# Kernel tuning notes

Hardware: AMD Instinct MI355X
Metric: run time of the kernel (lower is better)

Reference implementation:

```python
import jax, jax.numpy as jnp
import numpy as np

N_CLAUSES = 200000
N_FEATURES = 64
HIDDEN = 128
N_STEPS = 512


def setup_inputs() -> dict:
    key = jax.random.key(0)
    ks = jax.random.split(key, 8)
    features = jax.random.normal(ks[0], (N_CLAUSES, N_FEATURES), jnp.float32)
    W1 = jax.random.normal(ks[1], (N_FEATURES, HIDDEN), jnp.float32) / np.sqrt(N_FEATURES)
    b1 = jnp.zeros((HIDDEN,), jnp.float32)
    W2 = jax.random.normal(ks[2], (HIDDEN, HIDDEN), jnp.float32) / np.sqrt(HIDDEN)
    b2 = jnp.zeros((HIDDEN,), jnp.float32)
    key_w = jax.random.normal(ks[3], (HIDDEN,), jnp.float32) / np.sqrt(HIDDEN)
    # sel_mask[s, n] = clause n is in the passive set at SEL step s
    sel_mask = jax.random.bernoulli(ks[4], 0.5, (N_STEPS, N_CLAUSES))
    # proof_mask[n] = clause n participates in the final proof (sparse)
    proof_mask = jax.random.bernoulli(ks[5], 0.02, (N_CLAUSES,))
    # guarantee passive & proof nonempty at every step (torch code divides by its size)
    proof_mask = proof_mask.at[0].set(True)
    sel_mask = sel_mask.at[:, 0].set(True)
    return {
        "features": features, "W1": W1, "b1": b1, "W2": W2, "b2": b2,
        "key_w": key_w, "sel_mask": sel_mask, "proof_mask": proof_mask,
    }


def reference(features, W1, b1, W2, b2, key_w, sel_mask, proof_mask):
    # clause_embedder: 2-layer MLP; clause_key: dot with key vector -> one logit per clause
    h = jax.nn.relu(features @ W1 + b1)          # [N, H]
    emb = h @ W2 + b2                            # [N, H]
    logits = emb @ key_w                         # [N]

    neg = jnp.finfo(logits.dtype).min
    masked = jnp.where(sel_mask, logits[None, :], neg)   # [S, N]
    lse = jax.nn.logsumexp(masked, axis=1)                # [S] log-softmax denominator over passive set

    tgt = sel_mask & proof_mask[None, :]                  # [S, N] passive & proof
    cnt = tgt.sum(axis=1).astype(logits.dtype)            # [S] (>=1 by construction)
    # soft-target CE: -sum_j t_j * log_softmax(logits)_j, t uniform over tgt
    num = jnp.where(tgt, logits[None, :], 0.0).sum(axis=1) / cnt
    loss = (lse - num).mean()                             # mean over SEL steps
    return loss
```

## Files before the change

kernel.cpp:

```cpp
#include <hip/hip_runtime.h>
#include <hip/hip_bf16.h>

#define DEV __device__ __forceinline__

constexpr int NC = 200000;
constexpr int NF = 64;
constexpr int NH = 128;
constexpr int NS = 512;

constexpr int OF_CFG   = 0;
constexpr int OF_W1    = 16;
constexpr int OF_B1    = OF_W1 + NF * NH;
constexpr int OF_W2K   = OF_B1 + NH;
constexpr int OF_B2K   = OF_W2K + NH;
constexpr int OF_MAX   = OF_B2K + 1;
constexpr int OF_ACCE  = OF_MAX + 1;
constexpr int OF_ACCP  = OF_ACCE + NS;
constexpr int OF_ACCC  = OF_ACCP + NS;
constexpr int OF_LOGIT = 16384;
constexpr int OF_E     = OF_LOGIT + NC;
constexpr int OF_PL    = OF_E + NC;
constexpr int OF_PC    = OF_PL + NC;

DEV float bf2f(unsigned short u) { return __uint_as_float(((unsigned)u) << 16); }

DEV float loadF(const void* p, int i, int fk) {
    return fk ? bf2f(((const unsigned short*)p)[i]) : ((const float*)p)[i];
}

DEV unsigned flipf(float x) {
    unsigned u = __float_as_uint(x);
    return (u & 0x80000000u) ? ~u : (u | 0x80000000u);
}
DEV float unflipf(unsigned u) {
    unsigned b = (u & 0x80000000u) ? (u ^ 0x80000000u) : ~u;
    return __uint_as_float(b);
}

DEV bool okhalf(unsigned h) { return h == 0u || h == 1u || h == 0x3F80u || h == 0x3C00u; }

__global__ void k_probe(const void* features, const void* W1, const void* b1,
                        const void* W2, const void* b2, const void* keyw,
                        const void* sel, float* ws) {
    __shared__ int s_tiny, s_w4, s_w2;
    __shared__ float kw[NH];
    __shared__ float pr[NH];
    int tx = threadIdx.x;
    if (tx == 0) { s_tiny = 0; s_w4 = 1; s_w2 = 1; }
    __syncthreads();
    {
        const unsigned short* u = (const unsigned short*)features;
        unsigned e = (u[tx] >> 7) & 0xFFu;
        if (e < 100u) atomicAdd(&s_tiny, 1);
        const unsigned* w = (const unsigned*)sel;
        unsigned v = w[tx];
        if (!(v == 0u || v == 1u || v == 0x3F800000u)) atomicAnd(&s_w4, 0);
        if (!(okhalf(v & 0xFFFFu) && okhalf(v >> 16))) atomicAnd(&s_w2, 0);
    }
    __syncthreads();
    int fk = (s_tiny >= 8) ? 0 : 1;
    int mw = s_w4 ? 4 : (s_w2 ? 2 : 1);
    if (tx == 0) { ((int*)ws)[0] = fk; ((int*)ws)[1] = mw; }
    if (tx < NH) kw[tx] = loadF(keyw, tx, fk);
    for (int i = tx; i < NF * NH; i += blockDim.x) {
        int f = i >> 7;
        int j = i & (NH - 1);
        int jc = j >> 2, c = j & 3;
        ws[OF_W1 + ((jc * NF + f) << 2) + c] = loadF(W1, i, fk);
    }
    if (tx < NH) ws[OF_B1 + tx] = loadF(b1, tx, fk);
    __syncthreads();
    if (tx < NH) {
        float s = 0.f;
        for (int k = 0; k < NH; k++) s += loadF(W2, tx * NH + k, fk) * kw[k];
        ws[OF_W2K + tx] = s;
        pr[tx] = loadF(b2, tx, fk) * kw[tx];
    }
    __syncthreads();
    if (tx == 0) {
        float s = 0.f;
        for (int k = 0; k < NH; k++) s += pr[k];
        ws[OF_B2K] = s;
        ((unsigned*)ws)[OF_MAX] = 0u;
    }
    for (int i = tx; i < 3 * NS; i += blockDim.x) ws[OF_ACCE + i] = 0.f;
}

__global__ __launch_bounds__(256) void k_logits(const void* features,
                                                const float* __restrict__ w1t,
                                                const float* __restrict__ bias1,
                                                const float* __restrict__ wk,
                                                const float* __restrict__ cfg,
                                                float* __restrict__ logits,
                                                unsigned* __restrict__ maxp) {
    __shared__ float sred[4];
    int tx = threadIdx.x;
    int fk = ((const int*)cfg)[0];
    float b2k = cfg[OF_B2K];
    int n = blockIdx.x * 256 + tx;
    float acc = -3.0e38f;
    if (n < NC) {
        float feat[NF];
        if (fk) {
            const uint4* fp = (const uint4*)((const unsigned short*)features + (size_t)n * NF);
            #pragma unroll
            for (int q = 0; q < 8; q++) {
                uint4 v = fp[q];
                unsigned vv[4] = {v.x, v.y, v.z, v.w};
                #pragma unroll
                for (int h = 0; h < 4; h++) {
                    feat[q * 8 + h * 2 + 0] = __uint_as_float(vv[h] << 16);
                    feat[q * 8 + h * 2 + 1] = __uint_as_float(vv[h] & 0xFFFF0000u);
                }
            }
        } else {
            const float4* fp = (const float4*)((const float*)features + (size_t)n * NF);
            #pragma unroll
            for (int q = 0; q < 16; q++) {
                float4 v = fp[q];
                feat[q * 4 + 0] = v.x; feat[q * 4 + 1] = v.y;
                feat[q * 4 + 2] = v.z; feat[q * 4 + 3] = v.w;
            }
        }
        acc = b2k;
        for (int jc = 0; jc < NH / 4; jc++) {
            const float4* wp = (const float4*)(w1t + (size_t)jc * (NF * 4));
            float4 b = *(const float4*)(bias1 + jc * 4);
            float d0 = b.x, d1 = b.y, d2 = b.z, d3 = b.w;
            #pragma unroll
            for (int f = 0; f < NF; f++) {
                float4 w = wp[f];
                d0 += feat[f] * w.x; d1 += feat[f] * w.y;
                d2 += feat[f] * w.z; d3 += feat[f] * w.w;
            }
            float4 k4 = *(const float4*)(wk + jc * 4);
            acc += fmaxf(d0, 0.f) * k4.x + fmaxf(d1, 0.f) * k4.y
                 + fmaxf(d2, 0.f) * k4.z + fmaxf(d3, 0.f) * k4.w;
        }
        logits[n] = acc;
    }
    float m = acc;
    #pragma unroll
    for (int k = 1; k < 64; k <<= 1) m = fmaxf(m, __shfl_xor(m, k, 64));
    if ((tx & 63) == 0) sred[tx >> 6] = m;
    __syncthreads();
    if (tx == 0) {
        m = fmaxf(fmaxf(sred[0], sred[1]), fmaxf(sred[2], sred[3]));
        atomicMax(maxp, flipf(m));
    }
}

__global__ void k_prep(const void* proof, float* ws) {
    int n = blockIdx.x * 256 + threadIdx.x;
    if (n >= NC) return;
    int mw = ((const int*)ws)[1];
    float M = unflipf(((const unsigned*)ws)[OF_MAX]);
    float l = ws[OF_LOGIT + n];
    ws[OF_E + n] = __expf(l - M);
    bool pf;
    if (mw == 1)      pf = ((const unsigned char*)proof)[n] != 0;
    else if (mw == 2) pf = ((const unsigned short*)proof)[n] != 0;
    else              pf = ((const unsigned*)proof)[n] != 0;
    ws[OF_PL + n] = pf ? l : 0.f;
    ws[OF_PC + n] = pf ? 1.f : 0.f;
}

constexpr int NT_N = 16;
constexpr int BL_N = 256 * NT_N;
constexpr int SG = 32;

template<int MW>
DEV void bloop(const void* sel, int s0, int baddr,
               const float (&e)[NT_N], const float (&pl)[NT_N], const float (&pc)[NT_N],
               float* ws) {
    for (int si = 0; si < SG; si++) {
        int s = s0 + si;
        size_t off = (size_t)s * NC + (size_t)baddr;
        float m[NT_N];
        if (MW == 1) {
            uint4 w = *(const uint4*)((const unsigned char*)sel + off);
            unsigned v[4] = {w.x, w.y, w.z, w.w};
            #pragma unroll
            for (int q = 0; q < 4; q++)
                #pragma unroll
                for (int b = 0; b < 4; b++)
                    m[q * 4 + b] = ((v[q] >> (8 * b)) & 0xFFu) ? 1.f : 0.f;
        } else if (MW == 2) {
            const uint4* p = (const uint4*)((const unsigned short*)sel + off);
            #pragma unroll
            for (int h = 0; h < 2; h++) {
                uint4 w = p[h];
                unsigned v[4] = {w.x, w.y, w.z, w.w};
                #pragma unroll
                for (int q = 0; q < 4; q++) {
                    m[h * 8 + q * 2 + 0] = (v[q] & 0xFFFFu) ? 1.f : 0.f;
                    m[h * 8 + q * 2 + 1] = (v[q] >> 16) ? 1.f : 0.f;
                }
            }
        } else {
            const uint4* p = (const uint4*)((const unsigned*)sel + off);
            #pragma unroll
            for (int q = 0; q < 4; q++) {
                uint4 w = p[q];
                m[q * 4 + 0] = w.x ? 1.f : 0.f; m[q * 4 + 1] = w.y ? 1.f : 0.f;
                m[q * 4 + 2] = w.z ? 1.f : 0.f; m[q * 4 + 3] = w.w ? 1.f : 0.f;
            }
        }
        float se = 0.f, sp = 0.f, sc = 0.f;
        #pragma unroll
        for (int i = 0; i < NT_N; i++) {
            se += m[i] * e[i]; sp += m[i] * pl[i]; sc += m[i] * pc[i];
        }
        #pragma unroll
        for (int k = 1; k < 64; k <<= 1) {
            se += __shfl_xor(se, k, 64);
            sp += __shfl_xor(sp, k, 64);
            sc += __shfl_xor(sc, k, 64);
        }
        if ((threadIdx.x & 63) == 0) {
            atomicAdd(&ws[OF_ACCE + s], se);
            atomicAdd(&ws[OF_ACCP + s], sp);
            atomicAdd(&ws[OF_ACCC + s], sc);
        }
    }
}

__global__ __launch_bounds__(256) void k_phaseB(const void* sel, float* ws) {
    int tx = threadIdx.x;
    int base = blockIdx.x * BL_N + tx * NT_N;
    int s0 = blockIdx.y * SG;
    bool active = base < NC;
    int baddr = active ? base : 0;
    float e[NT_N], pl[NT_N], pc[NT_N];
    #pragma unroll
    for (int q = 0; q < 4; q++) {
        float4 ve = active ? ((const float4*)&ws[OF_E + baddr])[q]  : make_float4(0, 0, 0, 0);
        float4 vp = active ? ((const float4*)&ws[OF_PL + baddr])[q] : make_float4(0, 0, 0, 0);
        float4 vc = active ? ((const float4*)&ws[OF_PC + baddr])[q] : make_float4(0, 0, 0, 0);
        e[q * 4 + 0] = ve.x; e[q * 4 + 1] = ve.y; e[q * 4 + 2] = ve.z; e[q * 4 + 3] = ve.w;
        pl[q * 4 + 0] = vp.x; pl[q * 4 + 1] = vp.y; pl[q * 4 + 2] = vp.z; pl[q * 4 + 3] = vp.w;
        pc[q * 4 + 0] = vc.x; pc[q * 4 + 1] = vc.y; pc[q * 4 + 2] = vc.z; pc[q * 4 + 3] = vc.w;
    }
    int mw = ((const int*)ws)[1];
    if (mw == 1)      bloop<1>(sel, s0, baddr, e, pl, pc, ws);
    else if (mw == 2) bloop<2>(sel, s0, baddr, e, pl, pc, ws);
    else              bloop<4>(sel, s0, baddr, e, pl, pc, ws);
}

__global__ void k_final(float* ws, void* out) {
    __shared__ float sred[256];
    int tx = threadIdx.x;
    float M = unflipf(((const unsigned*)ws)[OF_MAX]);
    float sum = 0.f;
    for (int s = tx; s < NS; s += 256) {
        float lse = M + logf(ws[OF_ACCE + s]);
        sum += lse - ws[OF_ACCP + s] / ws[OF_ACCC + s];
    }
    sred[tx] = sum;
    __syncthreads();
    for (int k = 128; k > 0; k >>= 1) {
        if (tx < k) sred[tx] += sred[tx + k];
        __syncthreads();
    }
    if (tx == 0) {
        float loss = sred[0] / (float)NS;
        int fk = ((const int*)ws)[0];
        if (fk) ((__hip_bfloat16*)out)[0] = __float2bfloat16(loss);
        else    ((float*)out)[0] = loss;
    }
}

extern "C" void kernel_launch(void* const* d_in, const int* in_sizes, int n_in,
                              void* d_out, int out_size, void* d_ws, size_t ws_size,
                              hipStream_t stream) {
    const void* features = d_in[0];
    const void* W1   = d_in[1];
    const void* b1   = d_in[2];
    const void* W2   = d_in[3];
    const void* b2   = d_in[4];
    const void* keyw = d_in[5];
    const void* sel  = d_in[6];
    const void* proof = d_in[7];
    float* ws = (float*)d_ws;

    k_probe<<<1, 256, 0, stream>>>(features, W1, b1, W2, b2, keyw, sel, ws);
    int nblk = (NC + 255) / 256;
    k_logits<<<nblk, 256, 0, stream>>>(features, ws + OF_W1, ws + OF_B1, ws + OF_W2K,
                                       ws, ws + OF_LOGIT, (unsigned*)ws + OF_MAX);
    k_prep<<<nblk, 256, 0, stream>>>(proof, ws);
    dim3 gB((NC + BL_N - 1) / BL_N, NS / SG);
    k_phaseB<<<gB, 256, 0, stream>>>(sel, ws);
    k_final<<<1, 256, 0, stream>>>(ws, d_out);
}
```

Measured before the change: 699.9 us.

## Use bf16 MFMA for logits MLP and fuse prep into phase-B kernel

When features arrive as bf16, the first layer now runs on MFMA 16x16x32 bf16 instructions using a pre-swizzled W1 layout prepared in the probe kernel. Bias, ReLU and the W2·key projection are applied in the epilogue. The separate prep kernel is removed, so exp(logit-M) and the proof-mask terms are computed inside the phase-B kernel and the intermediate arrays are no longer written and reread. SG doubles to 64 steps per block, which halves how often per-block setup runs at the cost of fewer blocks. The fp32 fallback path is kept but only 64 of 256 threads work, and its bounds handling for the last block looks fragile.

```diff
diff --git a/kernel.cpp b/kernel.cpp
--- a/kernel.cpp
+++ b/kernel.cpp
@@ -7,6 +7,9 @@
 constexpr int NF = 64;
 constexpr int NH = 128;
 constexpr int NS = 512;
+
+typedef __attribute__((ext_vector_type(8))) short short8;
+typedef __attribute__((ext_vector_type(4))) float f32x4;
 
 constexpr int OF_CFG   = 0;
 constexpr int OF_W1    = 16;
@@ -17,17 +20,13 @@
 constexpr int OF_ACCE  = OF_MAX + 1;
 constexpr int OF_ACCP  = OF_ACCE + NS;
 constexpr int OF_ACCC  = OF_ACCP + NS;
+constexpr int OF_EPT   = OF_ACCC + NS;
 constexpr int OF_LOGIT = 16384;
-constexpr int OF_E     = OF_LOGIT + NC;
-constexpr int OF_PL    = OF_E + NC;
-constexpr int OF_PC    = OF_PL + NC;
 
 DEV float bf2f(unsigned short u) { return __uint_as_float(((unsigned)u) << 16); }
-
 DEV float loadF(const void* p, int i, int fk) {
     return fk ? bf2f(((const unsigned short*)p)[i]) : ((const float*)p)[i];
 }
-
 DEV unsigned flipf(float x) {
     unsigned u = __float_as_uint(x);
     return (u & 0x80000000u) ? ~u : (u | 0x80000000u);
@@ -36,7 +35,6 @@
     unsigned b = (u & 0x80000000u) ? (u ^ 0x80000000u) : ~u;
     return __uint_as_float(b);
 }
-
 DEV bool okhalf(unsigned h) { return h == 0u || h == 1u || h == 0x3F80u || h == 0x3C00u; }
 
 __global__ void k_probe(const void* features, const void* W1, const void* b1,
@@ -44,7 +42,7 @@
                         const void* sel, float* ws) {
     __shared__ int s_tiny, s_w4, s_w2;
     __shared__ float kw[NH];
-    __shared__ float pr[NH];
+    __shared__ float part[256];
     int tx = threadIdx.x;
     if (tx == 0) { s_tiny = 0; s_w4 = 1; s_w2 = 1; }
     __syncthreads();
@@ -62,112 +60,141 @@
     int mw = s_w4 ? 4 : (s_w2 ? 2 : 1);
     if (tx == 0) { ((int*)ws)[0] = fk; ((int*)ws)[1] = mw; }
     if (tx < NH) kw[tx] = loadF(keyw, tx, fk);
-    for (int i = tx; i < NF * NH; i += blockDim.x) {
-        int f = i >> 7;
-        int j = i & (NH - 1);
-        int jc = j >> 2, c = j & 3;
-        ws[OF_W1 + ((jc * NF + f) << 2) + c] = loadF(W1, i, fk);
+    if (fk) {
+        const unsigned short* w1u = (const unsigned short*)W1;
+        unsigned short* dstp = (unsigned short*)(ws + OF_W1);
+        for (int i = tx; i < NF * NH; i += blockDim.x) {
+            int k = i >> 7, col = i & 127;
+            int t = col >> 4, c = col & 15;
+            int ks = k >> 5, kr = k & 31, q = kr >> 3, j = kr & 7;
+            dstp[(((t * 2 + ks) * 64) + q * 16 + c) * 8 + j] = w1u[i];
+        }
+    } else {
+        for (int i = tx; i < NF * NH; i += blockDim.x) {
+            int f = i >> 7, j = i & (NH - 1);
+            int jc = j >> 2, c = j & 3;
+            ws[OF_W1 + ((jc * NF + f) << 2) + c] = loadF(W1, i, fk);
+        }
     }
     if (tx < NH) ws[OF_B1 + tx] = loadF(b1, tx, fk);
     __syncthreads();
-    if (tx < NH) {
+    {
+        int row = tx >> 1, half = tx & 1;
         float s = 0.f;
-        for (int k = 0; k < NH; k++) s += loadF(W2, tx * NH + k, fk) * kw[k];
-        ws[OF_W2K + tx] = s;
-        pr[tx] = loadF(b2, tx, fk) * kw[tx];
-    }
+        for (int k = half * 64; k < half * 64 + 64; k++)
+            s += loadF(W2, row * NH + k, fk) * kw[k];
+        part[tx] = s;
+    }
+    __syncthreads();
+    if (tx < NH) ws[OF_W2K + tx] = part[2 * tx] + part[2 * tx + 1];
+    __syncthreads();
+    if (tx < NH) part[tx] = loadF(b2, tx, fk) * kw[tx];
     __syncthreads();
     if (tx == 0) {
         float s = 0.f;
-        for (int k = 0; k < NH; k++) s += pr[k];
+        for (int k = 0; k < NH; k++) s += part[k];
         ws[OF_B2K] = s;
         ((unsigned*)ws)[OF_MAX] = 0u;
     }
+    __syncthreads();
+    if (tx < 128) {
+        int c = tx >> 3, t = tx & 7;
+        ws[OF_EPT + 2 * tx + 0] = ws[OF_B1 + 16 * t + c];
+        ws[OF_EPT + 2 * tx + 1] = ws[OF_W2K + 16 * t + c];
+    }
     for (int i = tx; i < 3 * NS; i += blockDim.x) ws[OF_ACCE + i] = 0.f;
 }
 
 __global__ __launch_bounds__(256) void k_logits(const void* features,
-                                                const float* __restrict__ w1t,
-                                                const float* __restrict__ bias1,
-                                                const float* __restrict__ wk,
-                                                const float* __restrict__ cfg,
+                                                const float* __restrict__ wsro,
                                                 float* __restrict__ logits,
                                                 unsigned* __restrict__ maxp) {
-    __shared__ float sred[4];
     int tx = threadIdx.x;
-    int fk = ((const int*)cfg)[0];
-    float b2k = cfg[OF_B2K];
-    int n = blockIdx.x * 256 + tx;
-    float acc = -3.0e38f;
-    if (n < NC) {
-        float feat[NF];
-        if (fk) {
-            const uint4* fp = (const uint4*)((const unsigned short*)features + (size_t)n * NF);
-            #pragma unroll
-            for (int q = 0; q < 8; q++) {
-                uint4 v = fp[q];
-                unsigned vv[4] = {v.x, v.y, v.z, v.w};
+    int fk = ((const int*)wsro)[0];
+    float b2k = wsro[OF_B2K];
+    if (fk) {
+        int wv = tx >> 6, l = tx & 63;
+        int m = l & 15, q = l >> 4;
+        int n0 = blockIdx.x * 64 + wv * 16;
+        const unsigned short* fb = (const unsigned short*)features + (size_t)n0 * NF;
+        short8 a0 = *(const short8*)(fb + m * NF + q * 8);
+        short8 a1 = *(const short8*)(fb + m * NF + q * 8 + 32);
+        const short8* bf = (const short8*)(const void*)(wsro + OF_W1);
+        f32x4 acc[8];
+        #pragma unroll
+        for (int t = 0; t < 8; t++) {
+            f32x4 z = {0.f, 0.f, 0.f, 0.f};
+            short8 b0 = bf[(t * 2 + 0) * 64 + l];
+            short8 b1f = bf[(t * 2 + 1) * 64 + l];
+            z = __builtin_amdgcn_mfma_f32_16x16x32_bf16(a0, b0, z, 0, 0, 0);
+            z = __builtin_amdgcn_mfma_f32_16x16x32_bf16(a1, b1f, z, 0, 0, 0);
+            acc[t] = z;
+        }
+        const float2* ep = (const float2*)(const void*)(wsro + OF_EPT) + m * 8;
+        float p[4] = {0.f, 0.f, 0.f, 0.f};
+        #pragma unroll
+        for (int t = 0; t < 8; t++) {
+            float2 bw = ep[t];
+            #pragma unroll
+            for (int r = 0; r < 4; r++)
+                p[r] += fmaxf(acc[t][r] + bw.x, 0.f) * bw.y;
+        }
+        #pragma unroll
+        for (int k = 1; k < 16; k <<= 1)
+            #pragma unroll
+            for (int r = 0; r < 4; r++) p[r] += __shfl_xor(p[r], k, 64);
+        float mx = -3.0e38f;
+        if (m == 0) {
+            float4 o;
+            o.x = p[0] + b2k; o.y = p[1] + b2k; o.z = p[2] + b2k; o.w = p[3] + b2k;
+            *(float4*)(logits + n0 + q * 4) = o;
+            mx = fmaxf(fmaxf(o.x, o.y), fmaxf(o.z, o.w));
+        }
+        #pragma unroll
+        for (int k = 1; k < 64; k <<= 1) mx = fmaxf(mx, __shfl_xor(mx, k, 64));
+        if (l == 0) atomicMax(maxp, flipf(mx));
+    } else {
+        const float* w1t = wsro + OF_W1;
+        const float* bias1 = wsro + OF_B1;
+        const float* wk = wsro + OF_W2K;
+        float acc = -3.0e38f;
+        int n = blockIdx.x * 64 + tx;
+        if (tx < 64 && n < NC) {
+            float feat[NF];
+            const float4* fp = (const float4*)((const float*)features + (size_t)n * NF);
+            #pragma unroll
+            for (int qq = 0; qq < 16; qq++) {
+                float4 v = fp[qq];
+                feat[qq * 4 + 0] = v.x; feat[qq * 4 + 1] = v.y;
+                feat[qq * 4 + 2] = v.z; feat[qq * 4 + 3] = v.w;
+            }
+            acc = b2k;
+            for (int jc = 0; jc < NH / 4; jc++) {
+                const float4* wp = (const float4*)(w1t + (size_t)jc * (NF * 4));
+                float4 b = *(const float4*)(bias1 + jc * 4);
+                float d0 = b.x, d1 = b.y, d2 = b.z, d3 = b.w;
                 #pragma unroll
-                for (int h = 0; h < 4; h++) {
-                    feat[q * 8 + h * 2 + 0] = __uint_as_float(vv[h] << 16);
-                    feat[q * 8 + h * 2 + 1] = __uint_as_float(vv[h] & 0xFFFF0000u);
+                for (int f = 0; f < NF; f++) {
+                    float4 w = wp[f];
+                    d0 += feat[f] * w.x; d1 += feat[f] * w.y;
+                    d2 += feat[f] * w.z; d3 += feat[f] * w.w;
                 }
-            }
-        } else {
-            const float4* fp = (const float4*)((const float*)features + (size_t)n * NF);
-            #pragma unroll
-            for (int q = 0; q < 16; q++) {
-                float4 v = fp[q];
-                feat[q * 4 + 0] = v.x; feat[q * 4 + 1] = v.y;
-                feat[q * 4 + 2] = v.z; feat[q * 4 + 3] = v.w;
-            }
-        }
-        acc = b2k;
-        for (int jc = 0; jc < NH / 4; jc++) {
-            const float4* wp = (const float4*)(w1t + (size_t)jc * (NF * 4));
-            float4 b = *(const float4*)(bias1 + jc * 4);
-            float d0 = b.x, d1 = b.y, d2 = b.z, d3 = b.w;
-            #pragma unroll
-            for (int f = 0; f < NF; f++) {
-                float4 w = wp[f];
-                d0 += feat[f] * w.x; d1 += feat[f] * w.y;
-                d2 += feat[f] * w.z; d3 += feat[f] * w.w;
-            }
-            float4 k4 = *(const float4*)(wk + jc * 4);
-            acc += fmaxf(d0, 0.f) * k4.x + fmaxf(d1, 0.f) * k4.y
-                 + fmaxf(d2, 0.f) * k4.z + fmaxf(d3, 0.f) * k4.w;
-        }
-        logits[n] = acc;
-    }
-    float m = acc;
-    #pragma unroll
-    for (int k = 1; k < 64; k <<= 1) m = fmaxf(m, __shfl_xor(m, k, 64));
-    if ((tx & 63) == 0) sred[tx >> 6] = m;
-    __syncthreads();
-    if (tx == 0) {
-        m = fmaxf(fmaxf(sred[0], sred[1]), fmaxf(sred[2], sred[3]));
-        atomicMax(maxp, flipf(m));
-    }
-}
-
-__global__ void k_prep(const void* proof, float* ws) {
-    int n = blockIdx.x * 256 + threadIdx.x;
-    if (n >= NC) return;
-    int mw = ((const int*)ws)[1];
-    float M = unflipf(((const unsigned*)ws)[OF_MAX]);
-    float l = ws[OF_LOGIT + n];
-    ws[OF_E + n] = __expf(l - M);
-    bool pf;
-    if (mw == 1)      pf = ((const unsigned char*)proof)[n] != 0;
-    else if (mw == 2) pf = ((const unsigned short*)proof)[n] != 0;
-    else              pf = ((const unsigned*)proof)[n] != 0;
-    ws[OF_PL + n] = pf ? l : 0.f;
-    ws[OF_PC + n] = pf ? 1.f : 0.f;
+                float4 k4 = *(const float4*)(wk + jc * 4);
+                acc += fmaxf(d0, 0.f) * k4.x + fmaxf(d1, 0.f) * k4.y
+                     + fmaxf(d2, 0.f) * k4.z + fmaxf(d3, 0.f) * k4.w;
+            }
+            logits[n] = acc;
+        }
+        float mm = acc;
+        #pragma unroll
+        for (int k = 1; k < 64; k <<= 1) mm = fmaxf(mm, __shfl_xor(mm, k, 64));
+        if ((tx & 63) == 0) atomicMax(maxp, flipf(mm));
+    }
 }
 
 constexpr int NT_N = 16;
 constexpr int BL_N = 256 * NT_N;
-constexpr int SG = 32;
+constexpr int SG = 64;
 
 template<int MW>
 DEV void bloop(const void* sel, int s0, int baddr,
@@ -184,7 +211,7 @@
             for (int q = 0; q < 4; q++)
                 #pragma unroll
                 for (int b = 0; b < 4; b++)
-                    m[q * 4 + b] = ((v[q] >> (8 * b)) & 0xFFu) ? 1.f : 0.f;
+                    m[q * 4 + b] = fminf((float)((v[q] >> (8 * b)) & 0xFFu), 1.0f);
         } else if (MW == 2) {
             const uint4* p = (const uint4*)((const unsigned short*)sel + off);
             #pragma unroll
@@ -225,23 +252,59 @@
     }
 }
 
-__global__ __launch_bounds__(256) void k_phaseB(const void* sel, float* ws) {
+__global__ __launch_bounds__(256) void k_phaseB(const void* sel, const void* proof,
+                                                const float* __restrict__ logits,
+                                                float* ws) {
     int tx = threadIdx.x;
     int base = blockIdx.x * BL_N + tx * NT_N;
     int s0 = blockIdx.y * SG;
     bool active = base < NC;
     int baddr = active ? base : 0;
+    float af = active ? 1.f : 0.f;
+    int mw = ((const int*)ws)[1];
+    float M = unflipf(((const unsigned*)ws)[OF_MAX]);
+    float lg[NT_N], pf[NT_N];
+    #pragma unroll
+    for (int q = 0; q < 4; q++) {
+        float4 v = ((const float4*)(logits + baddr))[q];
+        lg[q * 4 + 0] = v.x; lg[q * 4 + 1] = v.y; lg[q * 4 + 2] = v.z; lg[q * 4 + 3] = v.w;
+    }
+    if (mw == 1) {
+        uint4 w = *(const uint4*)((const unsigned char*)proof + baddr);
+        unsigned v[4] = {w.x, w.y, w.z, w.w};
+        #pragma unroll
+        for (int q = 0; q < 4; q++)
+            #pragma unroll
+            for (int b = 0; b < 4; b++)
+                pf[q * 4 + b] = fminf((float)((v[q] >> (8 * b)) & 0xFFu), 1.0f);
+    } else if (mw == 2) {
+        const uint4* p = (const uint4*)((const unsigned short*)proof + baddr);
+        #pragma unroll
+        for (int h = 0; h < 2; h++) {
+            uint4 w = p[h];
+            unsigned v[4] = {w.x, w.y, w.z, w.w};
+            #pragma unroll
+            for (int q = 0; q < 4; q++) {
+                pf[h * 8 + q * 2 + 0] = (v[q] & 0xFFFFu) ? 1.f : 0.f;
+                pf[h * 8 + q * 2 + 1] = (v[q] >> 16) ? 1.f : 0.f;
+            }
+        }
+    } else {
+        const uint4* p = (const uint4*)((const unsigned*)proof + baddr);
+        #pragma unroll
+        for (int q = 0; q < 4; q++) {
+            uint4 w = p[q];
+            pf[q * 4 + 0] = w.x ? 1.f : 0.f; pf[q * 4 + 1] = w.y ? 1.f : 0.f;
+            pf[q * 4 + 2] = w.z ? 1.f : 0.f; pf[q * 4 + 3] = w.w ? 1.f : 0.f;
+        }
+    }
     float e[NT_N], pl[NT_N], pc[NT_N];
     #pragma unroll
-    for (int q = 0; q < 4; q++) {
-        float4 ve = active ? ((const float4*)&ws[OF_E + baddr])[q]  : make_float4(0, 0, 0, 0);
-        float4 vp = active ? ((const float4*)&ws[OF_PL + baddr])[q] : make_float4(0, 0, 0, 0);
-        float4 vc = active ? ((const float4*)&ws[OF_PC + baddr])[q] : make_float4(0, 0, 0, 0);
-        e[q * 4 + 0] = ve.x; e[q * 4 + 1] = ve.y; e[q * 4 + 2] = ve.z; e[q * 4 + 3] = ve.w;
-        pl[q * 4 + 0] = vp.x; pl[q * 4 + 1] = vp.y; pl[q * 4 + 2] = vp.z; pl[q * 4 + 3] = vp.w;
-        pc[q * 4 + 0] = vc.x; pc[q * 4 + 1] = vc.y; pc[q * 4 + 2] = vc.z; pc[q * 4 + 3] = vc.w;
-    }
-    int mw = ((const int*)ws)[1];
+    for (int i = 0; i < NT_N; i++) {
+        e[i]  = af * __expf(lg[i] - M);
+        pl[i] = af * pf[i] * lg[i];
+        pc[i] = af * pf[i];
+    }
     if (mw == 1)      bloop<1>(sel, s0, baddr, e, pl, pc, ws);
     else if (mw == 2) bloop<2>(sel, s0, baddr, e, pl, pc, ws);
     else              bloop<4>(sel, s0, baddr, e, pl, pc, ws);
@@ -284,11 +347,9 @@
     float* ws = (float*)d_ws;
 
     k_probe<<<1, 256, 0, stream>>>(features, W1, b1, W2, b2, keyw, sel, ws);
-    int nblk = (NC + 255) / 256;
-    k_logits<<<nblk, 256, 0, stream>>>(features, ws + OF_W1, ws + OF_B1, ws + OF_W2K,
-                                       ws, ws + OF_LOGIT, (unsigned*)ws + OF_MAX);
-    k_prep<<<nblk, 256, 0, stream>>>(proof, ws);
+    k_logits<<<(NC + 63) / 64, 256, 0, stream>>>(features, ws, ws + OF_LOGIT,
+                                                 (unsigned*)ws + OF_MAX);
     dim3 gB((NC + BL_N - 1) / BL_N, NS / SG);
-    k_phaseB<<<gB, 256, 0, stream>>>(sel, ws);
+    k_phaseB<<<gB, 256, 0, stream>>>(sel, proof, ws + OF_LOGIT, ws);
     k_final<<<1, 256, 0, stream>>>(ws, d_out);
 }
```

Result: slower. 829.2 us (+18.5%).
